# Optimization experiments

Hardware: AMD Instinct MI355X
Metric: run time of the kernel (lower is better)

Reference implementation:

```python
import jax, jax.numpy as jnp
import numpy as np

EMBED_DIM = 1024
CONTEXT_LEN = 2048
NUM_HEADS = 16
HEAD_DIM = EMBED_DIM // NUM_HEADS
BATCH = 2
SEQ = 2048


def setup_inputs() -> dict:
    key = jax.random.key(0)
    ks = jax.random.split(key, 6)
    s = 1.0 / np.sqrt(EMBED_DIM)
    x = jax.random.normal(ks[0], (BATCH, SEQ, EMBED_DIM), dtype=jnp.float32)
    # nn.Linear weights stored as [out, in]; we keep [in, out] for x @ W
    W_q = jax.random.uniform(ks[1], (EMBED_DIM, EMBED_DIM), jnp.float32, -s, s)
    W_k = jax.random.uniform(ks[2], (EMBED_DIM, EMBED_DIM), jnp.float32, -s, s)
    W_v = jax.random.uniform(ks[3], (EMBED_DIM, EMBED_DIM), jnp.float32, -s, s)
    W_o = jax.random.uniform(ks[4], (EMBED_DIM, EMBED_DIM), jnp.float32, -s, s)
    b_o = jax.random.uniform(ks[5], (EMBED_DIM,), jnp.float32, -s, s)
    return {"x": x, "W_q": W_q, "W_k": W_k, "W_v": W_v, "W_o": W_o, "b_o": b_o}


def reference(x, W_q, W_k, W_v, W_o, b_o):
    b, s, _ = x.shape
    # project and split heads: [b, s, e] -> [b, h, s, d]
    def heads(t):
        return t.reshape(b, s, NUM_HEADS, HEAD_DIM).transpose(0, 2, 1, 3)
    q = heads(x @ W_q)
    k = heads(x @ W_k)
    v = heads(x @ W_v)
    scores = jnp.einsum("bhqd,bhkd->bhqk", q, k)  # full seq x seq scores
    causal = jnp.triu(jnp.ones((s, s), dtype=bool), k=1)
    scores = jnp.where(causal, -jnp.inf, scores)
    attn = jax.nn.softmax(scores / np.sqrt(HEAD_DIM).astype(np.float32), axis=-1)
    ctx = jnp.einsum("bhqk,bhkd->bhqd", attn, v)
    ctx = ctx.transpose(0, 2, 1, 3).reshape(b, s, EMBED_DIM)
    return ctx @ W_o + b_o
```

## Files before the change

kernel.cpp:

```cpp
#include <hip/hip_runtime.h>

#define EMBED 1024
#define SEQL  2048
#define NHEAD 16
#define HDIM  64
#define NBATCH 2
#define MROWS 4096

typedef __attribute__((ext_vector_type(4))) float  f32x4;
typedef __attribute__((ext_vector_type(8))) __bf16 bf16x8;

__device__ __forceinline__ short f2bf(float f){
  union { float f; unsigned u; } x; x.f = f;
  unsigned r = x.u + 0x7fffu + ((x.u >> 16) & 1u);
  return (short)(r >> 16);
}

#define GLDS(gp, lp) __builtin_amdgcn_global_load_lds( \
    (const __attribute__((address_space(1))) void*)(gp), \
    (__attribute__((address_space(3))) void*)(lp), 16, 0, 0)

#define WAITV(N) do { asm volatile("s_waitcnt vmcnt(" #N ")" ::: "memory"); \
                      __builtin_amdgcn_sched_barrier(0); } while(0)
#define BARRIER() do { __builtin_amdgcn_s_barrier(); \
                       __builtin_amdgcn_sched_barrier(0); } while(0)

__global__ __launch_bounds__(256) void prep_kernel(const float* __restrict__ x,
    const float* __restrict__ W0, const float* __restrict__ W1,
    const float* __restrict__ W2, const float* __restrict__ W3,
    short* __restrict__ Xb, short* __restrict__ WtAll){
  __shared__ float tile[32][33];
  const int z = blockIdx.z;
  if (z < 4){
    const float* W = (z==0)?W0:(z==1)?W1:(z==2)?W2:W3;
    short* Wt = WtAll + z*(EMBED*EMBED);
    const int bx = blockIdx.x*32, by = blockIdx.y*32;
    const int tx = threadIdx.x & 31, ty = threadIdx.x >> 5;
    #pragma unroll
    for (int i=0;i<32;i+=8) tile[ty+i][tx] = W[(by+ty+i)*EMBED + bx+tx];
    __syncthreads();
    #pragma unroll
    for (int i=0;i<32;i+=8) Wt[(bx+ty+i)*EMBED + by+tx] = f2bf(tile[tx][ty+i]);
  } else {
    const int blk = (z-4)*1024 + blockIdx.y*32 + blockIdx.x;
    const int i = (blk*256 + threadIdx.x)*4;
    float4 v = *(const float4*)(x + i);
    short4 o; o.x=f2bf(v.x); o.y=f2bf(v.y); o.z=f2bf(v.z); o.w=f2bf(v.w);
    *(short4*)(Xb + i) = o;
  }
}

__device__ __forceinline__ void gemm_tile_128(const short* __restrict__ A,
    const short* __restrict__ Bt, short* As, short* Bs, int m0, int n0, f32x4 acc[4][4]){
  const int tid  = threadIdx.x;
  const int lane = tid & 63;
  const int wid  = tid >> 6;
  const int wrow = (wid >> 1) * 64, wcol = (wid & 1) * 64;
  const int arow = tid >> 2, acol8 = (tid & 3) * 8;
  const int l15 = lane & 15, lg = lane >> 4;

  auto STAGE = [&](int b, int k0){
    short* as = As + b*4096;
    short* bs = Bs + b*4096;
    GLDS(A  + (m0      + arow) * 1024 + k0 + acol8, as + tid*8);
    GLDS(A  + (m0 + 64 + arow) * 1024 + k0 + acol8, as + 2048 + tid*8);
    GLDS(Bt + (n0      + arow) * 1024 + k0 + acol8, bs + tid*8);
    GLDS(Bt + (n0 + 64 + arow) * 1024 + k0 + acol8, bs + 2048 + tid*8);
  };

  STAGE(0, 0); STAGE(1, 32);
  WAITV(4);
  BARRIER();
  for (int k = 0; k < 32; ++k){
    if (k + 2 < 32) STAGE((k+2)%3, (k+2)*32);
    const short* as = As + (k%3)*4096;
    const short* bs = Bs + (k%3)*4096;
    bf16x8 a[4], b[4];
    #pragma unroll
    for (int i=0;i<4;++i) a[i] = *(const bf16x8*)(as + (wrow+16*i+l15)*32 + 8*lg);
    #pragma unroll
    for (int j=0;j<4;++j) b[j] = *(const bf16x8*)(bs + (wcol+16*j+l15)*32 + 8*lg);
    #pragma unroll
    for (int i=0;i<4;++i)
      #pragma unroll
      for (int j=0;j<4;++j)
        acc[i][j] = __builtin_amdgcn_mfma_f32_16x16x32_bf16(a[i], b[j], acc[i][j], 0,0,0);
    if (k + 2 < 32) { WAITV(4); } else { WAITV(0); }
    BARRIER();
  }
}

__device__ __forceinline__ void gemm_tile_64(const short* __restrict__ A,
    const short* __restrict__ Bt, short* As, short* Bs, int m0, int n0, f32x4 acc[2][4]){
  const int tid  = threadIdx.x;
  const int lane = tid & 63;
  const int wid  = tid >> 6;
  const int wrow = (wid >> 1) * 32, wcol = (wid & 1) * 64;
  const int arow = tid >> 2, acol8 = (tid & 3) * 8;
  const int l15 = lane & 15, lg = lane >> 4;

  auto STAGE = [&](int b, int k0){
    short* as = As + b*2048;
    short* bs = Bs + b*4096;
    GLDS(A  + (m0      + arow) * 1024 + k0 + acol8, as + tid*8);
    GLDS(Bt + (n0      + arow) * 1024 + k0 + acol8, bs + tid*8);
    GLDS(Bt + (n0 + 64 + arow) * 1024 + k0 + acol8, bs + 2048 + tid*8);
  };

  STAGE(0, 0); STAGE(1, 32);
  WAITV(3);
  BARRIER();
  for (int k = 0; k < 32; ++k){
    if (k + 2 < 32) STAGE((k+2)%3, (k+2)*32);
    const short* as = As + (k%3)*2048;
    const short* bs = Bs + (k%3)*4096;
    bf16x8 a[2], b[4];
    #pragma unroll
    for (int i=0;i<2;++i) a[i] = *(const bf16x8*)(as + (wrow+16*i+l15)*32 + 8*lg);
    #pragma unroll
    for (int j=0;j<4;++j) b[j] = *(const bf16x8*)(bs + (wcol+16*j+l15)*32 + 8*lg);
    #pragma unroll
    for (int i=0;i<2;++i)
      #pragma unroll
      for (int j=0;j<4;++j)
        acc[i][j] = __builtin_amdgcn_mfma_f32_16x16x32_bf16(a[i], b[j], acc[i][j], 0,0,0);
    if (k + 2 < 32) { WAITV(3); } else { WAITV(0); }
    BARRIER();
  }
}

__global__ __launch_bounds__(256) void gemm_qkv_kernel(const short* __restrict__ Xb,
    const short* __restrict__ WtAll, short* __restrict__ Q, short* __restrict__ K,
    short* __restrict__ Vt){
  __shared__ __align__(16) short SH[24576];
  short* As = SH;
  short* Bs = SH + 12288;
  const int m0 = blockIdx.x*128, n0 = blockIdx.y*128, z = blockIdx.z;
  const short* Bt = WtAll + z*(EMBED*EMBED);
  f32x4 acc[4][4] = {};
  gemm_tile_128(Xb, Bt, As, Bs, m0, n0, acc);
  const int tid  = threadIdx.x;
  const int lane = tid & 63;
  const int wid  = tid >> 6;
  const int wrow = (wid >> 1) * 64, wcol = (wid & 1) * 64;
  const int l15 = lane & 15, lg = lane >> 4;
  const int bb = m0 >> 11, srow0 = m0 & 2047;

  if (z < 2){
    short* out = z ? K : Q;
    const float qscl = (z==0) ? (0.125f * 1.44269504f) : 1.0f;
    #pragma unroll
    for (int i=0;i<4;++i)
      #pragma unroll
      for (int j=0;j<4;++j)
        #pragma unroll
        for (int r=0;r<4;++r){
          int m = m0 + wrow + 16*i + 4*lg + r;
          int n = n0 + wcol + 16*j + l15;
          int srow = m & 2047, hh = n >> 6, d = n & 63;
          out[(((bb<<4)+hh)*SEQL + srow)*HDIM + d] = f2bf(acc[i][j][r] * qscl);
        }
  } else {
    short* T = SH;
    #pragma unroll
    for (int i=0;i<4;++i)
      #pragma unroll
      for (int j=0;j<4;++j){
        int n_loc = wcol + 16*j + l15;
        int mb    = wrow + 16*i + 4*lg;
        short4 pk;
        pk.x = f2bf(acc[i][j][0]); pk.y = f2bf(acc[i][j][1]);
        pk.z = f2bf(acc[i][j][2]); pk.w = f2bf(acc[i][j][3]);
        *(short4*)(T + n_loc*128 + (mb ^ ((n_loc & 7) << 3))) = pk;
      }
    __syncthreads();
    #pragma unroll
    for (int it=0; it<8; ++it){
      int n_loc = 16*it + (tid >> 4);
      int mch   = (tid & 15) * 8;
      int4 v = *(const int4*)(T + n_loc*128 + (mch ^ ((n_loc & 7) << 3)));
      int n_glob = n0 + n_loc;
      int hh = n_glob >> 6, d = n_glob & 63;
      *(int4*)(Vt + (((bb<<4)+hh)*HDIM + d)*SEQL + srow0 + mch) = v;
    }
  }
}

__global__ __launch_bounds__(256) void gemm_out_kernel(const short* __restrict__ Ctx,
    const short* __restrict__ WtO, const float* __restrict__ bias, float* __restrict__ out){
  __shared__ __align__(16) short As[3*2048], Bs[3*4096];
  const int m0 = blockIdx.x*64, n0 = blockIdx.y*128;
  f32x4 acc[2][4] = {};
  gemm_tile_64(Ctx, WtO, As, Bs, m0, n0, acc);
  const int lane = threadIdx.x & 63;
  const int wid  = threadIdx.x >> 6;
  const int wrow = (wid >> 1) * 32, wcol = (wid & 1) * 64;
  const int l15 = lane & 15, lg = lane >> 4;
  #pragma unroll
  for (int i=0;i<2;++i)
    #pragma unroll
    for (int j=0;j<4;++j)
      #pragma unroll
      for (int r=0;r<4;++r){
        int m = m0 + wrow + 16*i + 4*lg + r;
        int n = n0 + wcol + 16*j + l15;
        out[m*EMBED + n] = acc[i][j][r] + bias[n];
      }
}

__global__ __launch_bounds__(512, 4) void attn_kernel(const short* __restrict__ Q,
    const short* __restrict__ K, const short* __restrict__ Vt, short* __restrict__ Ctx){
  __shared__ __align__(16) char lds[65536];
  const int tid  = threadIdx.x;
  const int lane = tid & 63;
  const int wid  = tid >> 6;
  const int bid   = blockIdx.x;
  const int xcd   = bid & 7;
  const int i7    = bid >> 3;
  const int bh    = xcd + 8*(i7 & 3);
  const int cidx  = i7 >> 2;
  const int chunk = (cidx < 8) ? cidx : 23 - cidx;
  const int q0blk = chunk * 128;
  const int ntblk = 2*chunk + 2;
  const int q0w   = q0blk + 16*wid;
  const int qlast = q0w + 15;

  const short* Qh  = Q  + bh*(SEQL*HDIM);
  const char*  KhB = (const char*)(K  + bh*(SEQL*HDIM));
  const char*  VhB = (const char*)(Vt + bh*(HDIM*SEQL));
  const int l15 = lane & 15, lg = lane >> 4;
  const int lg20 = 20 * lg;
  const int swE = (l15 & 7) << 3;
  const int swB = (l15 & 7) << 4;
  const int laneRow = lane >> 3;
  const int colSwz  = 16 * ((lane & 7) ^ laneRow);
  const int r0 = 8 * wid;

  const short* qp = Qh + (q0w + l15)*HDIM + 8*lg;
  bf16x8 bq0 = *(const bf16x8*)qp;
  bf16x8 bq1 = *(const bf16x8*)(qp + 32);

  f32x4 acc[4];
  #pragma unroll
  for (int j=0; j<4; ++j) acc[j] = (f32x4){0.f,0.f,0.f,0.f};
  float mrun = -3e30f, lrun = 0.f;

  short* pw = (short*)(lds + 49152 + wid*2048);

  auto STAGE = [&](int b, int t){
    char* kb = lds + b*16384;
    char* vb = kb + 8192;
    const int kv0 = t*64;
    GLDS(KhB + (kv0 + r0 + laneRow)*128 + colSwz, kb + r0*128);
    GLDS(VhB + (r0 + laneRow)*4096 + kv0*2 + colSwz, vb + r0*128);
  };

  STAGE(0, 0); STAGE(1, 1);
  WAITV(2);
  BARRIER();

  for (int t = 0; t < ntblk; ++t){
    const int kv0 = t*64;
    if (t + 2 < ntblk) STAGE((t+2)%3, t+2);
    if (kv0 <= qlast){
      const char* kb = lds + (t%3)*16384;
      const char* vb = kb + 8192;
      f32x4 sc[4];
      __builtin_amdgcn_s_setprio(1);
      #pragma unroll
      for (int c=0; c<4; ++c){
        const char* kr = kb + (16*c + l15)*128;
        bf16x8 k0 = *(const bf16x8*)(kr + ((16*lg) ^ swB));
        bf16x8 k1 = *(const bf16x8*)(kr + ((64 + 16*lg) ^ swB));
        f32x4 z = (f32x4){0.f,0.f,0.f,0.f};
        z = __builtin_amdgcn_mfma_f32_16x16x32_bf16(k0, bq0, z, 0,0,0);
        z = __builtin_amdgcn_mfma_f32_16x16x32_bf16(k1, bq1, z, 0,0,0);
        sc[c] = z;
      }
      __builtin_amdgcn_s_setprio(0);
      if (kv0 + 63 > q0w){
        #pragma unroll
        for (int c=0; c<4; ++c)
          #pragma unroll
          for (int r=0; r<4; ++r)
            if (kv0 + 16*c + 4*lg + r > q0w + l15) sc[c][r] = -3e30f;
      }
      float pm = -3e30f;
      #pragma unroll
      for (int c=0; c<4; ++c)
        #pragma unroll
        for (int r=0; r<4; ++r) pm = fmaxf(pm, sc[c][r]);
      pm = fmaxf(pm, __shfl_xor(pm, 16));
      pm = fmaxf(pm, __shfl_xor(pm, 32));
      const int resc = !__all(pm <= mrun);
      float mn = mrun, ss = 1.0f;
      if (resc){
        mn = fmaxf(mrun, pm);
        ss = __builtin_amdgcn_exp2f(mrun - mn);
        mrun = mn;
      }
      float ls = 0.f;
      #pragma unroll
      for (int c=0; c<4; ++c)
        #pragma unroll
        for (int r=0; r<4; ++r){
          float p = __builtin_amdgcn_exp2f(sc[c][r] - mn);
          sc[c][r] = p;
          ls += p;
        }
      ls += __shfl_xor(ls, 16);
      ls += __shfl_xor(ls, 32);
      if (resc){
        lrun = lrun*ss + ls;
        float srg[4];
        #pragma unroll
        for (int r=0; r<4; ++r) srg[r] = __shfl(ss, lg20 + r);
        #pragma unroll
        for (int j=0; j<4; ++j)
          #pragma unroll
          for (int r=0; r<4; ++r) acc[j][r] *= srg[r];
      } else {
        lrun += ls;
      }
      #pragma unroll
      for (int c=0; c<4; ++c){
        short4 pk;
        pk.x = f2bf(sc[c][0]); pk.y = f2bf(sc[c][1]);
        pk.z = f2bf(sc[c][2]); pk.w = f2bf(sc[c][3]);
        *(short4*)(pw + l15*64 + ((16*c + 4*lg) ^ swE)) = pk;
      }
      bf16x8 pa0 = *(const bf16x8*)(pw + l15*64 + ((8*lg)      ^ swE));
      bf16x8 pa1 = *(const bf16x8*)(pw + l15*64 + ((32 + 8*lg) ^ swE));
      __builtin_amdgcn_s_setprio(1);
      #pragma unroll
      for (int j=0; j<4; ++j){
        const char* vrp = vb + (16*j + l15)*128;
        bf16x8 v0 = *(const bf16x8*)(vrp + ((16*lg) ^ swB));
        bf16x8 v1 = *(const bf16x8*)(vrp + ((64 + 16*lg) ^ swB));
        acc[j] = __builtin_amdgcn_mfma_f32_16x16x32_bf16(pa0, v0, acc[j], 0,0,0);
        acc[j] = __builtin_amdgcn_mfma_f32_16x16x32_bf16(pa1, v1, acc[j], 0,0,0);
      }
      __builtin_amdgcn_s_setprio(0);
    }
    if (t + 2 < ntblk) { WAITV(2); } else { WAITV(0); }
    BARRIER();
  }

  const int bb = bh >> 4, hh = bh & 15;
  float lr[4];
  #pragma unroll
  for (int r=0; r<4; ++r) lr[r] = __builtin_amdgcn_rcpf(__shfl(lrun, lg20 + r));
  #pragma unroll
  for (int j=0; j<4; ++j)
    #pragma unroll
    for (int r=0; r<4; ++r){
      int qg = q0w + 4*lg + r;
      Ctx[(bb*SEQL + qg)*EMBED + hh*HDIM + 16*j + l15] = f2bf(acc[j][r] * lr[r]);
    }
}

extern "C" void kernel_launch(void* const* d_in, const int* in_sizes, int n_in,
                              void* d_out, int out_size, void* d_ws, size_t ws_size,
                              hipStream_t stream){
  const float* x  = (const float*)d_in[0];
  const float* Wq = (const float*)d_in[1];
  const float* Wk = (const float*)d_in[2];
  const float* Wv = (const float*)d_in[3];
  const float* Wo = (const float*)d_in[4];
  const float* bo = (const float*)d_in[5];
  float* out = (float*)d_out;

  char* ws = (char*)d_ws;
  const size_t MB = 1u << 20;
  short* Xb  = (short*)(ws +  0*MB);
  short* Wt  = (short*)(ws +  8*MB);
  short* Q   = (short*)(ws + 16*MB);
  short* Kk  = (short*)(ws + 24*MB);
  short* Vt  = (short*)(ws + 32*MB);
  short* Ctx = (short*)(ws + 40*MB);

  prep_kernel<<<dim3(32,32,8), 256, 0, stream>>>(x, Wq, Wk, Wv, Wo, Xb, Wt);
  gemm_qkv_kernel<<<dim3(32,8,3), 256, 0, stream>>>(Xb, Wt, Q, Kk, Vt);
  attn_kernel<<<512, 512, 0, stream>>>(Q, Kk, Vt, Ctx);
  gemm_out_kernel<<<dim3(64,8), 256, 0, stream>>>(Ctx, Wt + 3*(EMBED*EMBED), bo, out);
}
```

Measured before the change: 112.8 us.

## Switch attention K/V staging from triple to double buffering with tree reductions

Replaces the three-stage async K/V LDS ring with a two-buffer ping-pong, so per-block LDS drops from 64KB to 48KB and more blocks may fit per CU. The explicit vmcnt waits plus raw barriers become __syncthreads, and only one tile is prefetched ahead. Row max and sum reductions become tree-shaped to shorten dependency chains, and the manual bf16 rounding is replaced with a native cast. The cost is less load latency hiding, and __syncthreads may not wait on the global_load_lds vmcnt the way the explicit wait did.

```diff
diff --git a/kernel.cpp b/kernel.cpp
--- a/kernel.cpp
+++ b/kernel.cpp
@@ -11,9 +11,9 @@
 typedef __attribute__((ext_vector_type(8))) __bf16 bf16x8;
 
 __device__ __forceinline__ short f2bf(float f){
-  union { float f; unsigned u; } x; x.f = f;
-  unsigned r = x.u + 0x7fffu + ((x.u >> 16) & 1u);
-  return (short)(r >> 16);
+  __bf16 h = (__bf16)f;
+  union { __bf16 h; short s; } u; u.h = h;
+  return u.s;
 }
 
 #define GLDS(gp, lp) __builtin_amdgcn_global_load_lds( \
@@ -210,7 +210,7 @@
 
 __global__ __launch_bounds__(512, 4) void attn_kernel(const short* __restrict__ Q,
     const short* __restrict__ K, const short* __restrict__ Vt, short* __restrict__ Ctx){
-  __shared__ __align__(16) char lds[65536];
+  __shared__ __align__(16) char lds[49152];
   const int tid  = threadIdx.x;
   const int lane = tid & 63;
   const int wid  = tid >> 6;
@@ -245,7 +245,7 @@
   for (int j=0; j<4; ++j) acc[j] = (f32x4){0.f,0.f,0.f,0.f};
   float mrun = -3e30f, lrun = 0.f;
 
-  short* pw = (short*)(lds + 49152 + wid*2048);
+  short* pw = (short*)(lds + 32768 + wid*2048);
 
   auto STAGE = [&](int b, int t){
     char* kb = lds + b*16384;
@@ -255,15 +255,15 @@
     GLDS(VhB + (r0 + laneRow)*4096 + kv0*2 + colSwz, vb + r0*128);
   };
 
-  STAGE(0, 0); STAGE(1, 1);
-  WAITV(2);
-  BARRIER();
-
+  STAGE(0, 0);
+  __syncthreads();
+
+  int cur = 0;
   for (int t = 0; t < ntblk; ++t){
     const int kv0 = t*64;
-    if (t + 2 < ntblk) STAGE((t+2)%3, t+2);
+    if (t + 1 < ntblk) STAGE(cur ^ 1, t + 1);
     if (kv0 <= qlast){
-      const char* kb = lds + (t%3)*16384;
+      const char* kb = lds + cur*16384;
       const char* vb = kb + 8192;
       f32x4 sc[4];
       __builtin_amdgcn_s_setprio(1);
@@ -285,11 +285,11 @@
           for (int r=0; r<4; ++r)
             if (kv0 + 16*c + 4*lg + r > q0w + l15) sc[c][r] = -3e30f;
       }
-      float pm = -3e30f;
+      float cm[4];
       #pragma unroll
       for (int c=0; c<4; ++c)
-        #pragma unroll
-        for (int r=0; r<4; ++r) pm = fmaxf(pm, sc[c][r]);
+        cm[c] = fmaxf(fmaxf(sc[c][0], sc[c][1]), fmaxf(sc[c][2], sc[c][3]));
+      float pm = fmaxf(fmaxf(cm[0], cm[1]), fmaxf(cm[2], cm[3]));
       pm = fmaxf(pm, __shfl_xor(pm, 16));
       pm = fmaxf(pm, __shfl_xor(pm, 32));
       const int resc = !__all(pm <= mrun);
@@ -299,15 +299,16 @@
         ss = __builtin_amdgcn_exp2f(mrun - mn);
         mrun = mn;
       }
-      float ls = 0.f;
       #pragma unroll
       for (int c=0; c<4; ++c)
         #pragma unroll
-        for (int r=0; r<4; ++r){
-          float p = __builtin_amdgcn_exp2f(sc[c][r] - mn);
-          sc[c][r] = p;
-          ls += p;
-        }
+        for (int r=0; r<4; ++r)
+          sc[c][r] = __builtin_amdgcn_exp2f(sc[c][r] - mn);
+      float cs[4];
+      #pragma unroll
+      for (int c=0; c<4; ++c)
+        cs[c] = (sc[c][0] + sc[c][1]) + (sc[c][2] + sc[c][3]);
+      float ls = (cs[0] + cs[1]) + (cs[2] + cs[3]);
       ls += __shfl_xor(ls, 16);
       ls += __shfl_xor(ls, 32);
       if (resc){
@@ -342,8 +343,8 @@
       }
       __builtin_amdgcn_s_setprio(0);
     }
-    if (t + 2 < ntblk) { WAITV(2); } else { WAITV(0); }
-    BARRIER();
+    __syncthreads();
+    cur ^= 1;
   }
 
   const int bb = bh >> 4, hh = bh & 15;
```

Result: faster. 107.4 us (-4.7%).
